# Performance work log

Measured on AMD Instinct MI355X. Metric: run time of the kernel, lower is better.

Reference implementation:

```python
import jax, jax.numpy as jnp
import numpy as np

B, S, D, F, E, NS, K = 2, 2048, 512, 2048, 8, 2, 2


def setup_inputs() -> dict:
    key = jax.random.key(0)
    ks = jax.random.split(key, 6)
    scale = 0.02

    def p(k, shape):
        return jax.random.normal(k, shape, jnp.float32) * scale

    return {
        "x": jax.random.normal(ks[0], (B, S, D), jnp.float32),
        "gate_w": p(ks[1], (E, D)),
        "gate_b": jnp.zeros((E,), jnp.float32),
        "sw1": p(ks[2], (NS, F, D)),
        "sb1": jnp.zeros((NS, F), jnp.float32),
        "sw2": p(ks[3], (NS, D, F)),
        "sb2": jnp.zeros((NS, D), jnp.float32),
        "rw1": p(ks[4], (E, F, D)),
        "rb1": jnp.zeros((E, F), jnp.float32),
        "rw2": p(ks[5], (E, D, F)),
        "rb2": jnp.zeros((E, D), jnp.float32),
    }


def reference(x, gate_w, gate_b, sw1, sb1, sw2, sb2, rw1, rb1, rw2, rb2):
    b, s, d = x.shape
    t = x.reshape(-1, d)  # [T, D] flatten batch*seq tokens
    T = t.shape[0]

    # ---- shared experts: sum over NS FFNs (GELU exact, matching nn.GELU) ----
    hs = jax.nn.gelu(jnp.einsum('td,nfd->ntf', t, sw1) + sb1[:, None, :],
                     approximate=False)
    shared = jnp.einsum('ntf,ndf->td', hs, sw2) + sb2.sum(axis=0)

    # ---- router: softmax over experts, top-k probs/indices ----
    logits = t @ gate_w.T + gate_b               # [T, E]
    probs = jax.nn.softmax(logits, axis=-1)
    top_v, top_i = jax.lax.top_k(probs, K)       # [T, K]

    # combine weights: cw[t, e] = sum_k top_v[t, k] * (top_i[t, k] == e)
    cw = jnp.zeros_like(probs).at[jnp.arange(T)[:, None], top_i].add(top_v)  # [T, E]

    # ---- routed experts: run each expert FFN over all tokens, combine by cw ----
    # Mathematically identical to the masked gather/scatter loop in the source:
    # tokens with cw[t,e]==0 contribute nothing.
    hr = jax.nn.gelu(jnp.einsum('td,efd->etf', t, rw1) + rb1[:, None, :],
                     approximate=False)          # [E, T, F]
    oe = jnp.einsum('etf,edf->etd', hr, rw2) + rb2[:, None, :]  # [E, T, D]
    routed = jnp.einsum('etd,te->td', oe, cw)    # weighted combine

    return (shared + routed).reshape(b, s, d)
```

## Files before the change

### kernel.cpp

```cpp
#include <hip/hip_runtime.h>
#include <math.h>

typedef unsigned short u16;
typedef __attribute__((ext_vector_type(8))) __bf16 bf16x8;
typedef __attribute__((ext_vector_type(4))) float floatx4;

#define T_TOK 4096
#define DD    512
#define FF    2048
#define EE    8
#define NSH   2

#define BM 128
#define BN 128
#define BK 32
#define LDK 40
#define BT2 64
#define CAP 4096
#define PADF 0x80000000u
#define NSLOT (2 * T_TOK + EE * BM)

__device__ __forceinline__ float bf2f(u16 v) {
  union { unsigned int u; float f; } c; c.u = ((unsigned int)v) << 16; return c.f;
}
__device__ __forceinline__ u16 f2bf(float f) {
  union { float ff; unsigned int u; } c; c.ff = f;
  unsigned int u = c.u;
  u += 0x7fffu + ((u >> 16) & 1u);
  return (u16)(u >> 16);
}
__device__ __forceinline__ float decode(const void* p, size_t idx, int f) {
  return f ? ((const float*)p)[idx] : bf2f(((const u16*)p)[idx]);
}
__device__ __forceinline__ bf16x8 load8(const void* base, size_t idx, int f) {
  if (f) {
    const float* p = (const float*)base + idx;
    float4 a = *(const float4*)p;
    float4 b = *(const float4*)(p + 4);
    union { bf16x8 v; u16 s[8]; } u;
    u.s[0] = f2bf(a.x); u.s[1] = f2bf(a.y); u.s[2] = f2bf(a.z); u.s[3] = f2bf(a.w);
    u.s[4] = f2bf(b.x); u.s[5] = f2bf(b.y); u.s[6] = f2bf(b.z); u.s[7] = f2bf(b.w);
    return u.v;
  }
  return *(const bf16x8*)((const u16*)base + idx);
}
__device__ __forceinline__ void loadf8(const void* p, size_t idx, int f,
                                       float* o) {
  if (f) {
    const float* q = (const float*)p + idx;
    float4 a = *(const float4*)q;
    float4 b = *(const float4*)(q + 4);
    o[0] = a.x; o[1] = a.y; o[2] = a.z; o[3] = a.w;
    o[4] = b.x; o[5] = b.y; o[6] = b.z; o[7] = b.w;
  } else {
    union { bf16x8 v; u16 s[8]; } u;
    u.v = *(const bf16x8*)((const u16*)p + idx);
#pragma unroll
    for (int j = 0; j < 8; ++j) o[j] = bf2f(u.s[j]);
  }
}

__device__ __forceinline__ float fast_gelu(float v) {
  float x  = v * 0.70710678118654752f;
  float ax = fabsf(x);
  float t  = __builtin_amdgcn_rcpf(fmaf(0.3275911f, ax, 1.0f));
  float p  = fmaf(t, 1.061405429f, -1.453152027f);
  p = fmaf(t, p, 1.421413741f);
  p = fmaf(t, p, -0.284496736f);
  p = fmaf(t, p, 0.254829592f);
  p = p * t;
  float e  = __expf(-ax * ax);
  float er = fmaf(-p, e, 1.0f);
  er = (x < 0.f) ? -er : er;
  return 0.5f * v * (1.0f + er);
}

__device__ __forceinline__ void gll16(const void* g, void* l) {
  __builtin_amdgcn_global_load_lds(
      (const __attribute__((address_space(1))) void*)g,
      (__attribute__((address_space(3))) void*)l, 16, 0, 0);
}

#define BK2 64
__device__ __forceinline__ void core128swz(
    const u16* gA0, const u16* gA1, const u16* gA2, const u16* gA3,
    const u16* gB0, const u16* gB1, const u16* gB2, const u16* gB3,
    int K, u16* As, u16* Bs, floatx4 acc[4][4],
    int wave, int wm, int wn, int r, int q) {
  const int rs = r & 7;
  for (int k0 = 0; k0 < K; k0 += BK2) {
    __syncthreads();
    gll16(gA0 + k0, As + wave * 512);
    gll16(gA1 + k0, As + 2048 + wave * 512);
    gll16(gA2 + k0, As + 4096 + wave * 512);
    gll16(gA3 + k0, As + 6144 + wave * 512);
    gll16(gB0 + k0, Bs + wave * 512);
    gll16(gB1 + k0, Bs + 2048 + wave * 512);
    gll16(gB2 + k0, Bs + 4096 + wave * 512);
    gll16(gB3 + k0, Bs + 6144 + wave * 512);
    __syncthreads();
#pragma unroll
    for (int s = 0; s < 2; ++s) {
      bf16x8 af[4], bfr[4];
#pragma unroll
      for (int mi = 0; mi < 4; ++mi) {
        int R = wm + mi * 16 + r;
        int u = (s * 4 + q) ^ rs;
        af[mi] = *(const bf16x8*)(As + R * 64 + u * 8);
      }
#pragma unroll
      for (int ni = 0; ni < 4; ++ni) {
        int R = wn + ni * 16 + r;
        int u = (s * 4 + q) ^ rs;
        bfr[ni] = *(const bf16x8*)(Bs + R * 64 + u * 8);
      }
#pragma unroll
      for (int mi = 0; mi < 4; ++mi)
#pragma unroll
        for (int ni = 0; ni < 4; ++ni)
          acc[mi][ni] = __builtin_amdgcn_mfma_f32_16x16x32_bf16(
              af[mi], bfr[ni], acc[mi][ni], 0, 0, 0);
    }
  }
}

__global__ __launch_bounds__(256) void detect_kernel(
    const void* x, const void* gw, const void* sw1, const void* sw2,
    const void* rw1, const void* rw2, int* flags, int* meta) {
  __shared__ int cnt;
  __shared__ int sflags[6];
  const void* ptrs[6] = {x, gw, sw1, sw2, rw1, rw2};
  for (int tnum = 0; tnum < 6; ++tnum) {
    if (threadIdx.x == 0) cnt = 0;
    __syncthreads();
    const u16* p = (const u16*)ptrs[tnum];
    int local = 0;
    for (int i = threadIdx.x; i < 4096; i += 256) {
      unsigned ef = (p[i] >> 7) & 0xFFu;
      if (ef >= 0xE0u) ++local;
    }
    if (local) atomicAdd(&cnt, local);
    __syncthreads();
    if (threadIdx.x == 0) sflags[tnum] = (cnt >= 16) ? 1 : 0;
    __syncthreads();
  }
  if (threadIdx.x == 0) {
#pragma unroll
    for (int i = 0; i < 6; ++i) flags[i] = sflags[i];
    flags[6] = sflags[0];
    flags[7] = 0;
  }
  if (meta && threadIdx.x < 24) meta[threadIdx.x] = 0;
}

__global__ __launch_bounds__(256) void conv_kernel(
    const void* __restrict__ src, u16* __restrict__ dst,
    const int* __restrict__ flags, int idx, size_t n) {
  int f = flags[idx];
  if (!f) return;
  size_t i = ((size_t)blockIdx.x * 256 + threadIdx.x) * 8;
  if (i >= n) return;
  *(bf16x8*)(dst + i) = load8(src, i, f);
}

__global__ __launch_bounds__(256) void router_v(
    const void* __restrict__ x, const void* __restrict__ gw,
    const u16* __restrict__ gb, const int* __restrict__ flags,
    float* __restrict__ cw, int2* __restrict__ tix) {
  int wave = threadIdx.x >> 6, lane = threadIdx.x & 63;
  int t = blockIdx.x * 4 + wave;
  int fx = flags[0], fg = flags[1];
  float xf[8];
  loadf8(x, (size_t)t * DD + lane * 8, fx, xf);
  float acc[EE];
#pragma unroll
  for (int e = 0; e < EE; ++e) {
    float gf[8];
    loadf8(gw, (size_t)e * DD + lane * 8, fg, gf);
    float a = 0.f;
#pragma unroll
    for (int j = 0; j < 8; ++j) a = fmaf(xf[j], gf[j], a);
    acc[e] = a;
  }
#pragma unroll
  for (int e = 0; e < EE; ++e) {
    float v = acc[e];
#pragma unroll
    for (int off = 32; off > 0; off >>= 1) v += __shfl_xor(v, off, 64);
    acc[e] = v;
  }
  if (lane == 0) {
    float m = -1e30f;
#pragma unroll
    for (int e = 0; e < EE; ++e) {
      acc[e] += bf2f(gb[e]);
      m = fmaxf(m, acc[e]);
    }
    float p[EE], s = 0.f;
#pragma unroll
    for (int e = 0; e < EE; ++e) { p[e] = expf(acc[e] - m); s += p[e]; }
    int i1 = 0;
#pragma unroll
    for (int e = 1; e < EE; ++e) if (p[e] > p[i1]) i1 = e;
    int i2 = (i1 == 0) ? 1 : 0;
#pragma unroll
    for (int e = 0; e < EE; ++e)
      if (e != i1 && p[e] > p[i2]) i2 = e;
    float inv = 1.0f / s;
#pragma unroll
    for (int e = 0; e < EE; ++e)
      cw[t * EE + e] = (e == i1 || e == i2) ? p[e] * inv : 0.0f;
    tix[t] = make_int2(i1, i2);
  }
}

__global__ __launch_bounds__(256) void build_lists(
    const int2* __restrict__ tix, int* __restrict__ meta,
    unsigned* __restrict__ list, int4* __restrict__ srec) {
  int t = blockIdx.x * 256 + threadIdx.x;
  if (t >= T_TOK) return;
  int2 ii = tix[t];
  int p0 = atomicAdd(&meta[ii.x], 1);
  list[(size_t)ii.x * CAP + p0] = (unsigned)t;
  int p1 = atomicAdd(&meta[ii.y], 1);
  list[(size_t)ii.y * CAP + p1] = (unsigned)t;
  srec[t] = make_int4(ii.x, p0, ii.y, p1);
}
__global__ __launch_bounds__(256) void pad_lists(int* meta, unsigned* list) {
  if (threadIdx.x == 0) {
    int off = 0;
    for (int e = 0; e < EE; ++e) {
      int c = meta[e];
      int pc = (c + BM - 1) & ~(BM - 1);
      meta[8 + e] = pc;
      meta[16 + e] = off;
      off += pc;
    }
  }
  __syncthreads();
#pragma unroll
  for (int e = 0; e < EE; ++e) {
    int c = meta[e], pc = meta[8 + e];
    int i = c + threadIdx.x;
    if (i < pc) list[(size_t)e * CAP + i] = PADF;
  }
}


__global__ __launch_bounds__(256) void g1_fused(
    const void* __restrict__ xr, const u16* __restrict__ xb,
    const void* __restrict__ s1r, const u16* __restrict__ s1b,
    const u16* __restrict__ sb1,
    const void* __restrict__ r1r, const u16* __restrict__ r1b,
    const u16* __restrict__ rb1, const unsigned* __restrict__ list,
    const int* __restrict__ meta, const int* __restrict__ flags,
    u16* __restrict__ Hsh, u16* __restrict__ Hrt) {
  const u16* xp  = flags[0] ? xb  : (const u16*)xr;
  const u16* s1p = flags[2] ? s1b : (const u16*)s1r;
  const u16* r1p = flags[4] ? r1b : (const u16*)r1r;

  int z = blockIdx.z;
  int bm = blockIdx.y * BM;
  int tid = threadIdx.x, lane = tid & 63, wave = tid >> 6;
  int wm = (wave >> 1) * 64, wn = (wave & 1) * 64;
  int r = lane & 15, q = lane >> 4;
  const int K = DD;

  int rsub = tid >> 3;
  int us = (tid & 7) ^ (rsub & 7);

  __shared__ u16 As[BM * BK2];
  __shared__ u16 Bs[BN * BK2];

  const u16 *gA[4], *gB[4];
  int e = 0, ho = 0, bn;
  if (z < 2) {
    bn = (z * 16 + blockIdx.x) * BN;
#pragma unroll
    for (int c = 0; c < 4; ++c) {
      gA[c] = xp + (size_t)(bm + c * 32 + rsub) * K + us * 8;
      gB[c] = s1p + (size_t)(bn + c * 32 + rsub) * K + us * 8;
    }
  } else {
    e = z - 2;
    if (bm >= meta[8 + e]) return;
    ho = meta[16 + e];
    bn = blockIdx.x * BN;
#pragma unroll
    for (int c = 0; c < 4; ++c) {
      unsigned tk = list[(size_t)e * CAP + bm + c * 32 + rsub] & 0x7fffffffu;
      gA[c] = xp + (size_t)tk * K + us * 8;
      gB[c] = r1p + (size_t)e * FF * DD + (size_t)(bn + c * 32 + rsub) * K +
              us * 8;
    }
  }

  floatx4 acc[4][4];
  floatx4 zero = {0.f, 0.f, 0.f, 0.f};
#pragma unroll
  for (int i = 0; i < 4; ++i)
#pragma unroll
    for (int j = 0; j < 4; ++j) acc[i][j] = zero;

  core128swz(gA[0], gA[1], gA[2], gA[3], gB[0], gB[1], gB[2], gB[3],
             K, As, Bs, acc, wave, wm, wn, r, q);

  if (z < 2) {
#pragma unroll
    for (int mi = 0; mi < 4; ++mi)
#pragma unroll
      for (int ni = 0; ni < 4; ++ni) {
        int col = bn + wn + ni * 16 + r;
        float bv = bf2f(sb1[col]);
#pragma unroll
        for (int rr = 0; rr < 4; ++rr) {
          int row = bm + wm + mi * 16 + q * 4 + rr;
          float v = acc[mi][ni][rr] + bv;
          Hsh[(size_t)row * (NSH * FF) + col] = f2bf(fast_gelu(v));
        }
      }
  } else {
#pragma unroll
    for (int mi = 0; mi < 4; ++mi)
#pragma unroll
      for (int ni = 0; ni < 4; ++ni) {
        int col = bn + wn + ni * 16 + r;
        float bv = bf2f(rb1[(size_t)e * FF + col]);
#pragma unroll
        for (int rr = 0; rr < 4; ++rr) {
          int slot = bm + wm + mi * 16 + q * 4 + rr;
          float v = acc[mi][ni][rr] + bv;
          Hrt[(size_t)(ho + slot) * FF + col] = f2bf(fast_gelu(v));
        }
      }
  }
}

__global__ __launch_bounds__(256) void g2_fused(
    const u16* __restrict__ Hsh,
    const void* __restrict__ s2r, const u16* __restrict__ s2b,
    const u16* __restrict__ sb2, const u16* __restrict__ Hrt,
    const void* __restrict__ r2r, const u16* __restrict__ r2b,
    const u16* __restrict__ rb2,
    const unsigned* __restrict__ list, const int* __restrict__ meta,
    const int* __restrict__ flags, const float* __restrict__ cw,
    float* __restrict__ oacc, float* __restrict__ Ort) {
  const u16* s2p = flags[3] ? s2b : (const u16*)s2r;
  const u16* r2p = flags[5] ? r2b : (const u16*)r2r;

  int z = blockIdx.z;
  int bm = blockIdx.y * BM;
  int bn = blockIdx.x * BN;
  int tid = threadIdx.x, lane = tid & 63, wave = tid >> 6;
  int wm = (wave >> 1) * 64, wn = (wave & 1) * 64;
  int r = lane & 15, q = lane >> 4;
  const int K = FF;

  int rsub = tid >> 3;
  int us = (tid & 7) ^ (rsub & 7);

  __shared__ u16 As[BM * BK2];
  __shared__ u16 Bs[BN * BK2];

  const u16 *gA[4], *gB[4];
  int e = 0, ho = 0;
  if (z < NSH) {
    const int ldA = NSH * FF;
#pragma unroll
    for (int c = 0; c < 4; ++c) {
      gA[c] = Hsh + (size_t)(bm + c * 32 + rsub) * ldA + (size_t)z * FF +
              us * 8;
      gB[c] = s2p + (size_t)z * DD * FF + (size_t)(bn + c * 32 + rsub) * K +
              us * 8;
    }
  } else {
    e = z - NSH;
    if (bm >= meta[8 + e]) return;
    ho = meta[16 + e];
#pragma unroll
    for (int c = 0; c < 4; ++c) {
      gA[c] = Hrt + (size_t)(ho + bm + c * 32 + rsub) * K + us * 8;
      gB[c] = r2p + (size_t)e * DD * FF + (size_t)(bn + c * 32 + rsub) * K +
              us * 8;
    }
  }

  floatx4 acc[4][4];
  floatx4 zero = {0.f, 0.f, 0.f, 0.f};
#pragma unroll
  for (int i = 0; i < 4; ++i)
#pragma unroll
    for (int j = 0; j < 4; ++j) acc[i][j] = zero;

  core128swz(gA[0], gA[1], gA[2], gA[3], gB[0], gB[1], gB[2], gB[3],
             K, As, Bs, acc, wave, wm, wn, r, q);

  if (z < NSH) {
    float* op = oacc + (size_t)z * T_TOK * DD;
#pragma unroll
    for (int mi = 0; mi < 4; ++mi)
#pragma unroll
      for (int ni = 0; ni < 4; ++ni) {
        int col = bn + wn + ni * 16 + r;
        float bv = bf2f(sb2[(size_t)z * DD + col]);
#pragma unroll
        for (int rr = 0; rr < 4; ++rr) {
          int row = bm + wm + mi * 16 + q * 4 + rr;
          op[(size_t)row * DD + col] = acc[mi][ni][rr] + bv;
        }
      }
  } else {
#pragma unroll
    for (int mi = 0; mi < 4; ++mi)
#pragma unroll
      for (int rr = 0; rr < 4; ++rr) {
        int slot = bm + wm + mi * 16 + q * 4 + rr;
        unsigned raw = list[(size_t)e * CAP + slot];
        if (raw & PADF) continue;
        float s = cw[raw * EE + e];
#pragma unroll
        for (int ni = 0; ni < 4; ++ni) {
          int col = bn + wn + ni * 16 + r;
          float v = acc[mi][ni][rr] + bf2f(rb2[(size_t)e * DD + col]);
          Ort[(size_t)(ho + slot) * DD + col] = s * v;
        }
      }
  }
}

typedef struct { u16 a, b, c, d; } u16x4;
__global__ __launch_bounds__(256) void combine_out(
    const float* __restrict__ oacc, const float* __restrict__ Ort,
    const int4* __restrict__ srec, const int* __restrict__ meta,
    void* __restrict__ out, const int* __restrict__ flags) {
  int t  = blockIdx.x * 2 + (threadIdx.x >> 7);
  int c4 = (threadIdx.x & 127) * 4;
  int4 sr = srec[t];
  int g0 = meta[16 + sr.x] + sr.y;
  int g1 = meta[16 + sr.z] + sr.w;
  float4 a = *(const float4*)(oacc + (size_t)t * DD + c4);
  float4 b = *(const float4*)(oacc + (size_t)(T_TOK + t) * DD + c4);
  float4 u = *(const float4*)(Ort + (size_t)g0 * DD + c4);
  float4 v = *(const float4*)(Ort + (size_t)g1 * DD + c4);
  float o0 = a.x + b.x + u.x + v.x;
  float o1 = a.y + b.y + u.y + v.y;
  float o2 = a.z + b.z + u.z + v.z;
  float o3 = a.w + b.w + u.w + v.w;
  size_t idx = (size_t)t * DD + c4;
  if (flags[6]) {
    *(float4*)((float*)out + idx) = make_float4(o0, o1, o2, o3);
  } else {
    u16x4 h = {f2bf(o0), f2bf(o1), f2bf(o2), f2bf(o3)};
    *(u16x4*)((u16*)out + idx) = h;
  }
}

__device__ __forceinline__ void gemm_core(const void* A, size_t aoff, int fA,
                                          const void* B, size_t boff, int fB,
                                          int K, u16* As, u16* Bs,
                                          floatx4 acc[4][4]) {
  int tid  = threadIdx.x;
  int lane = tid & 63, wave = tid >> 6;
  int wm = (wave >> 1) * 64, wn = (wave & 1) * 64;
  int r = lane & 15, q = lane >> 4;
  int srow = tid >> 2;
  int sc8  = (tid & 3) * 8;
  size_t abase = aoff + (size_t)srow * K + sc8;
  size_t bbase = boff + (size_t)srow * K + sc8;
  const size_t half = (size_t)64 * K;

  for (int k0 = 0; k0 < K; k0 += BK) {
    bf16x8 av0 = load8(A, abase + k0, fA);
    bf16x8 av1 = load8(A, abase + half + k0, fA);
    bf16x8 bv0 = load8(B, bbase + k0, fB);
    bf16x8 bv1 = load8(B, bbase + half + k0, fB);
    __syncthreads();
    *(bf16x8*)(As + srow * LDK + sc8)        = av0;
    *(bf16x8*)(As + (srow + 64) * LDK + sc8) = av1;
    *(bf16x8*)(Bs + srow * LDK + sc8)        = bv0;
    *(bf16x8*)(Bs + (srow + 64) * LDK + sc8) = bv1;
    __syncthreads();

    bf16x8 af[4], bfr[4];
#pragma unroll
    for (int mi = 0; mi < 4; ++mi)
      af[mi] = *(const bf16x8*)(As + (wm + mi * 16 + r) * LDK + q * 8);
#pragma unroll
    for (int ni = 0; ni < 4; ++ni)
      bfr[ni] = *(const bf16x8*)(Bs + (wn + ni * 16 + r) * LDK + q * 8);
#pragma unroll
    for (int mi = 0; mi < 4; ++mi)
#pragma unroll
      for (int ni = 0; ni < 4; ++ni)
        acc[mi][ni] = __builtin_amdgcn_mfma_f32_16x16x32_bf16(
            af[mi], bfr[ni], acc[mi][ni], 0, 0, 0);
  }
}

__global__ __launch_bounds__(256) void gemm1_gelu(
    const void* __restrict__ A, size_t aoff, const void* __restrict__ B,
    size_t boff, const u16* __restrict__ bias, size_t bioff,
    u16* __restrict__ H, const int* __restrict__ flags, int iA, int iB,
    int N, int K) {
  __shared__ u16 As[BM * LDK];
  __shared__ u16 Bs[BN * LDK];
  int fA = flags[iA], fB = flags[iB];
  floatx4 acc[4][4];
  floatx4 zero = {0.f, 0.f, 0.f, 0.f};
#pragma unroll
  for (int i = 0; i < 4; ++i)
#pragma unroll
    for (int j = 0; j < 4; ++j) acc[i][j] = zero;

  int bm = blockIdx.y * BM, bn = blockIdx.x * BN;
  gemm_core(A, aoff + (size_t)bm * K, fA, B, boff + (size_t)bn * K, fB, K,
            As, Bs, acc);

  int tid = threadIdx.x, wave = tid >> 6, lane = tid & 63;
  int wm = (wave >> 1) * 64, wn = (wave & 1) * 64;
  int r = lane & 15, q = lane >> 4;
#pragma unroll
  for (int mi = 0; mi < 4; ++mi)
#pragma unroll
    for (int ni = 0; ni < 4; ++ni) {
      int col = bn + wn + ni * 16 + r;
      float bv = bf2f(bias[bioff + col]);
#pragma unroll
      for (int rr = 0; rr < 4; ++rr) {
        int row = bm + wm + mi * 16 + q * 4 + rr;
        float v = acc[mi][ni][rr] + bv;
        H[(size_t)row * N + col] = f2bf(fast_gelu(v));
      }
    }
}

__global__ __launch_bounds__(256) void gemm2_acc(
    const u16* __restrict__ A, const void* __restrict__ B, size_t boff,
    const u16* __restrict__ bias, size_t bioff, float* __restrict__ outf,
    void* __restrict__ outb, const float* __restrict__ cw,
    const int* __restrict__ flags, int iB, int expert, int accum,
    int row0, int N, int K) {
  __shared__ u16 As[BT2 * LDK];
  __shared__ u16 Bs[BT2 * LDK];
  int fB = flags[iB], fO = flags[6];
  floatx4 acc[2][2];
  floatx4 zero = {0.f, 0.f, 0.f, 0.f};
#pragma unroll
  for (int i = 0; i < 2; ++i)
#pragma unroll
    for (int j = 0; j < 2; ++j) acc[i][j] = zero;

  int bm = blockIdx.y * BT2, bn = blockIdx.x * BT2;
  int tid  = threadIdx.x;
  int lane = tid & 63, wave = tid >> 6;
  int wm = (wave >> 1) * 32, wn = (wave & 1) * 32;
  int r = lane & 15, q = lane >> 4;
  int srow = tid >> 2;
  int sc8  = (tid & 3) * 8;
  size_t abase = (size_t)(bm + srow) * K + sc8;
  size_t bbase = boff + (size_t)(bn + srow) * K + sc8;

  for (int k0 = 0; k0 < K; k0 += BK) {
    bf16x8 av = *(const bf16x8*)(A + abase + k0);
    bf16x8 bv = load8(B, bbase + k0, fB);
    __syncthreads();
    *(bf16x8*)(As + srow * LDK + sc8) = av;
    *(bf16x8*)(Bs + srow * LDK + sc8) = bv;
    __syncthreads();

    bf16x8 af[2], bfr[2];
#pragma unroll
    for (int mi = 0; mi < 2; ++mi)
      af[mi] = *(const bf16x8*)(As + (wm + mi * 16 + r) * LDK + q * 8);
#pragma unroll
    for (int ni = 0; ni < 2; ++ni)
      bfr[ni] = *(const bf16x8*)(Bs + (wn + ni * 16 + r) * LDK + q * 8);
#pragma unroll
    for (int mi = 0; mi < 2; ++mi)
#pragma unroll
      for (int ni = 0; ni < 2; ++ni)
        acc[mi][ni] = __builtin_amdgcn_mfma_f32_16x16x32_bf16(
            af[mi], bfr[ni], acc[mi][ni], 0, 0, 0);
  }

#pragma unroll
  for (int mi = 0; mi < 2; ++mi)
#pragma unroll
    for (int rr = 0; rr < 4; ++rr) {
      int grow = row0 + bm + wm + mi * 16 + q * 4 + rr;
      float s = cw ? cw[grow * EE + expert] : 1.0f;
#pragma unroll
      for (int ni = 0; ni < 2; ++ni) {
        int col = bn + wn + ni * 16 + r;
        float v = acc[mi][ni][rr] + bf2f(bias[bioff + col]);
        size_t idx = (size_t)grow * N + col;
        if (outf) {
          float prev = accum ? outf[idx] : 0.0f;
          outf[idx] = prev + s * v;
        } else if (fO) {
          float* ob = (float*)outb;
          float prev = accum ? ob[idx] : 0.0f;
          ob[idx] = prev + s * v;
        } else {
          u16* ob = (u16*)outb;
          float prev = accum ? bf2f(ob[idx]) : 0.0f;
          ob[idx] = f2bf(prev + s * v);
        }
      }
    }
}

__global__ __launch_bounds__(256) void convert_out(
    const float* __restrict__ acc, void* __restrict__ out,
    const int* __restrict__ flags, int n) {
  int i = blockIdx.x * blockDim.x + threadIdx.x;
  if (i >= n) return;
  if (flags[6]) ((float*)out)[i] = acc[i];
  else ((u16*)out)[i] = f2bf(acc[i]);
}

extern "C" void kernel_launch(void* const* d_in, const int* in_sizes, int n_in,
                              void* d_out, int out_size, void* d_ws, size_t ws_size,
                              hipStream_t stream) {
  (void)in_sizes; (void)n_in; (void)out_size;
  const void* x   = d_in[0];
  const void* gw  = d_in[1];
  const u16*  gb  = (const u16*)d_in[2];
  const void* sw1 = d_in[3];
  const u16*  sb1 = (const u16*)d_in[4];
  const void* sw2 = d_in[5];
  const u16*  sb2 = (const u16*)d_in[6];
  const void* rw1 = d_in[7];
  const u16*  rb1 = (const u16*)d_in[8];
  const void* rw2 = d_in[9];
  const u16*  rb2 = (const u16*)d_in[10];

  const size_t NX   = (size_t)T_TOK * DD;
  const size_t NW1S = (size_t)NSH * FF * DD;
  const size_t NW1R = (size_t)EE * FF * DD;
  const size_t NW2S = (size_t)NSH * DD * FF;
  const size_t NW2R = (size_t)EE * DD * FF;

  size_t off = 0;
  const size_t flO   = off; off += 256;
  const size_t cwO   = off; off += (size_t)T_TOK * EE * 4;
  const size_t tixO  = off; off += (size_t)T_TOK * 8;
  const size_t metaO = off; off += 256;
  const size_t listO = off; off += (size_t)EE * CAP * 4;
  const size_t srecO = off; off += (size_t)T_TOK * 16;
  const size_t accO  = off; off += (size_t)NSH * T_TOK * DD * 4;
  const size_t hshO  = off; off += (size_t)T_TOK * NSH * FF * 2;
  const size_t hrtO  = off; off += (size_t)NSLOT * FF * 2;
  const size_t ortO  = off; off += (size_t)NSLOT * DD * 4;
  const size_t xbO   = off; off += NX * 2;
  const size_t s1O   = off; off += NW1S * 2;
  const size_t r1O   = off; off += NW1R * 2;
  const size_t s2O   = off; off += NW2S * 2;
  const size_t r2O   = off; off += NW2R * 2;
  const int fast = (off <= ws_size) ? 1 : 0;

  char* ws = (char*)d_ws;
  int*   flags = (int*)(ws + flO);
  float* cw    = (float*)(ws + cwO);
  dim3 blk(256);

  if (fast) {
    int2*     tix  = (int2*)(ws + tixO);
    int*      meta = (int*)(ws + metaO);
    unsigned* list = (unsigned*)(ws + listO);
    int4*     srec = (int4*)(ws + srecO);
    float*    oacc = (float*)(ws + accO);
    u16*      Hsh  = (u16*)(ws + hshO);
    u16*      Hrt  = (u16*)(ws + hrtO);
    float*    Ort  = (float*)(ws + ortO);
    u16*      xb   = (u16*)(ws + xbO);
    u16*      s1b  = (u16*)(ws + s1O);
    u16*      r1b  = (u16*)(ws + r1O);
    u16*      s2b  = (u16*)(ws + s2O);
    u16*      r2b  = (u16*)(ws + r2O);

    detect_kernel<<<1, 256, 0, stream>>>(x, gw, sw1, sw2, rw1, rw2, flags,
                                         meta);
    conv_kernel<<<NX   / 2048, 256, 0, stream>>>(x,   xb,  flags, 0, NX);
    conv_kernel<<<NW1S / 2048, 256, 0, stream>>>(sw1, s1b, flags, 2, NW1S);
    conv_kernel<<<NW1R / 2048, 256, 0, stream>>>(rw1, r1b, flags, 4, NW1R);
    conv_kernel<<<NW2S / 2048, 256, 0, stream>>>(sw2, s2b, flags, 3, NW2S);
    conv_kernel<<<NW2R / 2048, 256, 0, stream>>>(rw2, r2b, flags, 5, NW2R);
    router_v<<<T_TOK / 4, 256, 0, stream>>>(x, gw, gb, flags, cw, tix);
    build_lists<<<T_TOK / 256, 256, 0, stream>>>(tix, meta, list, srec);
    pad_lists<<<1, 256, 0, stream>>>(meta, list);

    dim3 gf1(16, T_TOK / BM, 2 + EE);
    g1_fused<<<gf1, blk, 0, stream>>>(x, xb, sw1, s1b, sb1, rw1, r1b, rb1,
                                      list, meta, flags, Hsh, Hrt);
    dim3 gf2(DD / BN, CAP / BM, NSH + EE);
    g2_fused<<<gf2, blk, 0, stream>>>(Hsh, sw2, s2b, sb2, Hrt, rw2, r2b, rb2,
                                      list, meta, flags, cw, oacc, Ort);
    combine_out<<<T_TOK / 2, 256, 0, stream>>>(oacc, Ort, srec, meta, d_out,
                                               flags);
    return;
  }

  detect_kernel<<<1, 256, 0, stream>>>(x, gw, sw1, sw2, rw1, rw2, flags,
                                       nullptr);
  const size_t flB = 256, cwB = (size_t)T_TOK * EE * 4, tixB = (size_t)T_TOK * 8;
  const size_t accB = (size_t)T_TOK * DD * 4;
  static const int tcs[4] = {4096, 2048, 1024, 512};
  int TC = 0, use_f32 = 1;
  for (int i = 0; i < 4; ++i)
    if (flB + cwB + tixB + accB + (size_t)tcs[i] * FF * 2 <= ws_size) { TC = tcs[i]; break; }
  if (!TC) {
    use_f32 = 0;
    for (int i = 0; i < 4; ++i)
      if (flB + cwB + tixB + (size_t)tcs[i] * FF * 2 <= ws_size) { TC = tcs[i]; break; }
  }
  if (!TC) { TC = 512; use_f32 = 0; }

  int2*  tix     = (int2*)(ws + flB + cwB);
  float* out_acc = use_f32 ? (float*)(ws + flB + cwB + tixB) : nullptr;
  u16*   H       = (u16*)(ws + flB + cwB + tixB + (use_f32 ? accB : 0));

  router_v<<<T_TOK / 4, 256, 0, stream>>>(x, gw, gb, flags, cw, tix);
  dim3 g1(FF / BN, TC / BM);
  dim3 g2(DD / BT2, TC / BT2);
  const int nchunk = T_TOK / TC;
  for (int f = 0; f < NSH + EE; ++f) {
    const void *w1, *w2; const u16 *b1, *b2; const float* cwp;
    int expert, i1, i2v; size_t w1off, w2off, b1off, b2off;
    if (f < NSH) {
      w1 = sw1; w2 = sw2; b1 = sb1; b2 = sb2;
      w1off = (size_t)f * FF * DD; w2off = (size_t)f * DD * FF;
      b1off = (size_t)f * FF; b2off = (size_t)f * DD;
      cwp = nullptr; expert = 0; i1 = 2; i2v = 3;
    } else {
      int e = f - NSH;
      w1 = rw1; w2 = rw2; b1 = rb1; b2 = rb2;
      w1off = (size_t)e * FF * DD; w2off = (size_t)e * DD * FF;
      b1off = (size_t)e * FF; b2off = (size_t)e * DD;
      cwp = cw; expert = e; i1 = 4; i2v = 5;
    }
    int accum = (f > 0) ? 1 : 0;
    for (int c = 0; c < nchunk; ++c) {
      size_t t0 = (size_t)c * TC;
      gemm1_gelu<<<g1, blk, 0, stream>>>(x, t0 * DD, w1, w1off, b1, b1off, H,
                                         flags, 0, i1, FF, DD);
      gemm2_acc<<<g2, blk, 0, stream>>>(H, w2, w2off, b2, b2off, out_acc,
                                        d_out, cwp, flags, i2v, expert, accum,
                                        (int)t0, DD, FF);
    }
  }
  if (use_f32)
    convert_out<<<(T_TOK * DD) / 256, 256, 0, stream>>>(out_acc, d_out, flags,
                                                        T_TOK * DD);
}
```

Before: 375.5 us.

## Merge conversion and list-building launches and remap GEMM block order

```diff
diff --git a/kernel.cpp b/kernel.cpp
--- a/kernel.cpp
+++ b/kernel.cpp
@@ -153,13 +153,32 @@
   if (meta && threadIdx.x < 24) meta[threadIdx.x] = 0;
 }
 
-__global__ __launch_bounds__(256) void conv_kernel(
-    const void* __restrict__ src, u16* __restrict__ dst,
-    const int* __restrict__ flags, int idx, size_t n) {
-  int f = flags[idx];
+#define U8_X  (T_TOK * DD / 8)
+#define U8_S1 (NSH * FF * DD / 8)
+#define U8_R1 (EE * FF * DD / 8)
+#define U8_S2 (NSH * DD * FF / 8)
+#define U8_R2 (EE * DD * FF / 8)
+#define U8_C0 (U8_X)
+#define U8_C1 (U8_C0 + U8_S1)
+#define U8_C2 (U8_C1 + U8_R1)
+#define U8_C3 (U8_C2 + U8_S2)
+#define U8_C4 (U8_C3 + U8_R2)
+__global__ __launch_bounds__(256) void conv_all(
+    const void* __restrict__ x, const void* __restrict__ sw1,
+    const void* __restrict__ rw1, const void* __restrict__ sw2,
+    const void* __restrict__ rw2, u16* __restrict__ xb,
+    u16* __restrict__ s1b, u16* __restrict__ r1b, u16* __restrict__ s2b,
+    u16* __restrict__ r2b, const int* __restrict__ flags) {
+  size_t u = (size_t)blockIdx.x * 256 + threadIdx.x;
+  const void* src; u16* dst; int fi; size_t base;
+  if (u < U8_C0)      { src = x;   dst = xb;  fi = 0; base = 0; }
+  else if (u < U8_C1) { src = sw1; dst = s1b; fi = 2; base = U8_C0; }
+  else if (u < U8_C2) { src = rw1; dst = r1b; fi = 4; base = U8_C1; }
+  else if (u < U8_C3) { src = sw2; dst = s2b; fi = 3; base = U8_C2; }
+  else                { src = rw2; dst = r2b; fi = 5; base = U8_C3; }
+  int f = flags[fi];
   if (!f) return;
-  size_t i = ((size_t)blockIdx.x * 256 + threadIdx.x) * 8;
-  if (i >= n) return;
+  size_t i = (u - base) * 8;
   *(bf16x8*)(dst + i) = load8(src, i, f);
 }
 
@@ -214,19 +233,18 @@
   }
 }
 
-__global__ __launch_bounds__(256) void build_lists(
+__global__ __launch_bounds__(1024) void build_pad(
     const int2* __restrict__ tix, int* __restrict__ meta,
     unsigned* __restrict__ list, int4* __restrict__ srec) {
-  int t = blockIdx.x * 256 + threadIdx.x;
-  if (t >= T_TOK) return;
-  int2 ii = tix[t];
-  int p0 = atomicAdd(&meta[ii.x], 1);
-  list[(size_t)ii.x * CAP + p0] = (unsigned)t;
-  int p1 = atomicAdd(&meta[ii.y], 1);
-  list[(size_t)ii.y * CAP + p1] = (unsigned)t;
-  srec[t] = make_int4(ii.x, p0, ii.y, p1);
-}
-__global__ __launch_bounds__(256) void pad_lists(int* meta, unsigned* list) {
+  for (int t = threadIdx.x; t < T_TOK; t += 1024) {
+    int2 ii = tix[t];
+    int p0 = atomicAdd(&meta[ii.x], 1);
+    list[(size_t)ii.x * CAP + p0] = (unsigned)t;
+    int p1 = atomicAdd(&meta[ii.y], 1);
+    list[(size_t)ii.y * CAP + p1] = (unsigned)t;
+    srec[t] = make_int4(ii.x, p0, ii.y, p1);
+  }
+  __syncthreads();
   if (threadIdx.x == 0) {
     int off = 0;
     for (int e = 0; e < EE; ++e) {
@@ -241,8 +259,8 @@
 #pragma unroll
   for (int e = 0; e < EE; ++e) {
     int c = meta[e], pc = meta[8 + e];
-    int i = c + threadIdx.x;
-    if (i < pc) list[(size_t)e * CAP + i] = PADF;
+    for (int i = c + threadIdx.x; i < pc; i += 1024)
+      list[(size_t)e * CAP + i] = PADF;
   }
 }
 
@@ -259,8 +277,12 @@
   const u16* s1p = flags[2] ? s1b : (const u16*)s1r;
   const u16* r1p = flags[4] ? r1b : (const u16*)r1r;
 
-  int z = blockIdx.z;
-  int bm = blockIdx.y * BM;
+  int L  = blockIdx.x + 16 * (blockIdx.y + 32 * blockIdx.z);
+  int xx = (L & 127) >> 3;
+  int pp = ((L >> 7) << 3) | (L & 7);
+  int z  = pp >> 5;
+  int bm = (pp & 31) * BM;
+
   int tid = threadIdx.x, lane = tid & 63, wave = tid >> 6;
   int wm = (wave >> 1) * 64, wn = (wave & 1) * 64;
   int r = lane & 15, q = lane >> 4;
@@ -275,7 +297,7 @@
   const u16 *gA[4], *gB[4];
   int e = 0, ho = 0, bn;
   if (z < 2) {
-    bn = (z * 16 + blockIdx.x) * BN;
+    bn = (z * 16 + xx) * BN;
 #pragma unroll
     for (int c = 0; c < 4; ++c) {
       gA[c] = xp + (size_t)(bm + c * 32 + rsub) * K + us * 8;
@@ -285,7 +307,7 @@
     e = z - 2;
     if (bm >= meta[8 + e]) return;
     ho = meta[16 + e];
-    bn = blockIdx.x * BN;
+    bn = xx * BN;
 #pragma unroll
     for (int c = 0; c < 4; ++c) {
       unsigned tk = list[(size_t)e * CAP + bm + c * 32 + rsub] & 0x7fffffffu;
@@ -348,9 +370,13 @@
   const u16* s2p = flags[3] ? s2b : (const u16*)s2r;
   const u16* r2p = flags[5] ? r2b : (const u16*)r2r;
 
-  int z = blockIdx.z;
-  int bm = blockIdx.y * BM;
-  int bn = blockIdx.x * BN;
+  int L  = blockIdx.x + 4 * (blockIdx.y + 32 * blockIdx.z);
+  int xx = (L & 31) >> 3;
+  int pp = ((L >> 5) << 3) | (L & 7);
+  int z  = pp >> 5;
+  int bm = (pp & 31) * BM;
+  int bn = xx * BN;
+
   int tid = threadIdx.x, lane = tid & 63, wave = tid >> 6;
   int wm = (wave >> 1) * 64, wn = (wave & 1) * 64;
   int r = lane & 15, q = lane >> 4;
@@ -681,14 +707,10 @@
 
     detect_kernel<<<1, 256, 0, stream>>>(x, gw, sw1, sw2, rw1, rw2, flags,
                                          meta);
-    conv_kernel<<<NX   / 2048, 256, 0, stream>>>(x,   xb,  flags, 0, NX);
-    conv_kernel<<<NW1S / 2048, 256, 0, stream>>>(sw1, s1b, flags, 2, NW1S);
-    conv_kernel<<<NW1R / 2048, 256, 0, stream>>>(rw1, r1b, flags, 4, NW1R);
-    conv_kernel<<<NW2S / 2048, 256, 0, stream>>>(sw2, s2b, flags, 3, NW2S);
-    conv_kernel<<<NW2R / 2048, 256, 0, stream>>>(rw2, r2b, flags, 5, NW2R);
+    conv_all<<<U8_C4 / 256, 256, 0, stream>>>(x, sw1, rw1, sw2, rw2, xb, s1b,
+                                              r1b, s2b, r2b, flags);
     router_v<<<T_TOK / 4, 256, 0, stream>>>(x, gw, gb, flags, cw, tix);
-    build_lists<<<T_TOK / 256, 256, 0, stream>>>(tix, meta, list, srec);
-    pad_lists<<<1, 256, 0, stream>>>(meta, list);
+    build_pad<<<1, 1024, 0, stream>>>(tix, meta, list, srec);
 
     dim3 gf1(16, T_TOK / BM, 2 + EE);
     g1_fused<<<gf1, blk, 0, stream>>>(x, xb, sw1, s1b, sb1, rw1, r1b, rb1,
```

New measurement: 374.7 us. About the same (-0.2%).
